# Optimization experiments

Hardware: AMD Instinct MI355X
Metric: run time of the kernel (lower is better)

## Reference

```python
import jax, jax.numpy as jnp
import numpy as np

B = 2_097_152  # batch (even, pairs are (0,1),(2,3),...)
C = 25         # hardcoded: M = eye(25), logits have 25 classes
LAMDA = 0.01


def setup_inputs() -> dict:
    key = jax.random.key(0)
    k1, k2 = jax.random.split(key, 2)
    inputs = jax.random.normal(k1, (B, C), dtype=jnp.float32)
    labels = jax.random.randint(k2, (B,), 0, C)
    M = jnp.eye(C, dtype=jnp.float32)  # learned Mahalanobis matrix (init = identity, as in torch)
    return {"inputs": inputs, "labels": labels, "M": M}


def _loss(inputs, M, labels):
    # ---- metric_learning: pairs (2i, 2i+1) ----
    a, b = inputs[0::2], inputs[1::2]          # [P, C]
    la, lb = labels[0::2], labels[1::2]        # [P]
    d = jnp.abs(a - b)                         # [P, C]
    # ||M.T * d[:,None]||_F = sqrt(sum_i d[i]^2 * sum_j M[j,i]^2)
    colsq = jnp.sum(M * M, axis=0)             # [C]
    norms = jnp.sqrt((d * d) @ colsq)          # [P]

    same = la == lb                            # positive pair mask
    pos = jnp.where(same, norms, jnp.zeros_like(norms))
    distance_p = jnp.sum(pos)
    # Faithful to source bug: distance_n is OVERWRITTEN (not accumulated) on each
    # negative pair as distance_p_so_far + norm; final value comes from the LAST
    # negative pair (0 if none exist).
    excl_cum_p = jnp.cumsum(pos) - pos         # distance_p before each pair
    neg_vals = excl_cum_p + norms              # candidate distance_n per pair
    P = norms.shape[0]
    last_neg = jnp.max(jnp.where(~same, jnp.arange(P), -1))
    distance_n = jnp.where(last_neg >= 0,
                           jnp.take(neg_vals, jnp.maximum(last_neg, 0)),
                           jnp.float32(0.0))
    metric_loss = jax.nn.relu(1.0 + distance_p - distance_n)

    # ---- cross entropy (mean over batch) ----
    logp = jax.nn.log_softmax(inputs, axis=-1)                       # [B, C]
    ce = -jnp.mean(jnp.take_along_axis(logp, labels[:, None], axis=-1))

    return ce + LAMDA * metric_loss / 2.0


def reference(inputs, labels, M):
    return _loss(inputs, M, labels)
```

## Files before the change

kernel.cpp:

```cpp
#include <hip/hip_runtime.h>
#include <math.h>

namespace {

constexpr int C      = 25;
constexpr int ROWS   = 256;
constexpr int TILE_F = ROWS * C;
constexpr int NBLK   = 512;

typedef const __attribute__((address_space(1))) void* gp_t;
typedef __attribute__((address_space(3))) void* lp_t;

__device__ __forceinline__ void load16_lds(const float* g, float* l) {
  __builtin_amdgcn_global_load_lds((gp_t)g, (lp_t)l, 16, 0, 2);
}

__global__ __launch_bounds__(256)
void k_ce(const float* __restrict__ x, const int* __restrict__ labels, int B,
          double* __restrict__ ce_part, int* __restrict__ ln_part) {
  __shared__ float tile[2][TILE_F];
  __shared__ float wsum[4];
  __shared__ int   wmax[4];

  const int t      = threadIdx.x;
  const int ntiles = B / ROWS;
  const int tpb    = ntiles / NBLK;
  const int ti0    = blockIdx.x * tpb;
  const int ti1    = min(ti0 + tpb, ntiles);

  float ce_local = 0.f;
  int   best     = -1;
  int   cur      = 0;

  int lab = 0;
  if (ti0 < ti1) {
    const float* g = x + (size_t)ti0 * TILE_F;
#pragma unroll
    for (int k = 0; k < 6; ++k)
      load16_lds(g + (k * 256 + t) * 4, &tile[0][(k * 256 + t) * 4]);
    if (t < 64) load16_lds(g + (1536 + t) * 4, &tile[0][(1536 + t) * 4]);
    lab = labels[(size_t)ti0 * ROWS + t];
  }

  for (int ti = ti0; ti < ti1; ++ti) {
    __syncthreads();

    const int tnext = ti + 1;
    int labn = 0;
    if (tnext < ti1) {
      const float* g = x + (size_t)tnext * TILE_F;
      float* buf = tile[cur ^ 1];
#pragma unroll
      for (int k = 0; k < 6; ++k)
        load16_lds(g + (k * 256 + t) * 4, &buf[(k * 256 + t) * 4]);
      if (t < 64) load16_lds(g + (1536 + t) * 4, &buf[(1536 + t) * 4]);
      labn = labels[(size_t)tnext * ROWS + t];
    }

    const float* r = &tile[cur][t * C];
    float e[C];
#pragma unroll
    for (int c = 0; c < C; ++c) e[c] = r[c];

    float m = e[0];
#pragma unroll
    for (int c = 1; c < C; ++c) m = fmaxf(m, e[c]);
    float s = 0.f, xl = 0.f;
#pragma unroll
    for (int c = 0; c < C; ++c) {
      s += __expf(e[c] - m);
      xl = (c == lab) ? e[c] : xl;
    }
    ce_local += (m + __logf(s)) - xl;

    const int nxt = __shfl_down(lab, 1, 64);
    if (((t & 1) == 0) && lab != nxt) best = ((ti * ROWS) + t) >> 1;

    lab = labn;
    cur ^= 1;
  }

#pragma unroll
  for (int off = 32; off; off >>= 1) {
    ce_local += __shfl_down(ce_local, off, 64);
    best = max(best, __shfl_down(best, off, 64));
  }
  const int lane = t & 63, wid = t >> 6;
  if (lane == 0) { wsum[wid] = ce_local; wmax[wid] = best; }
  __syncthreads();
  if (t == 0) {
    ce_part[blockIdx.x] = (double)((wsum[0] + wsum[1]) + (wsum[2] + wsum[3]));
    ln_part[blockIdx.x] = max(max(wmax[0], wmax[1]), max(wmax[2], wmax[3]));
  }
}

__global__ __launch_bounds__(256)
void k_fin(const float* __restrict__ x, const float* __restrict__ M,
           const double* __restrict__ ce_part, const int* __restrict__ ln_part,
           int P, int B, float* __restrict__ out) {
  __shared__ float  colsq[C];
  __shared__ double sred[4];
  __shared__ int    ired[4];
  __shared__ double tred[4];
  __shared__ int    s_last;

  const int t = threadIdx.x, lane = t & 63, wid = t >> 6;

  if (t < C) {
    float s = 0.f;
    for (int r = 0; r < C; ++r) {
      float m = M[r * C + t];
      s += m * m;
    }
    colsq[t] = s;
  }

  double ce = 0.0;
  int ln = -1;
  for (int i = t; i < NBLK; i += 256) {
    ce += ce_part[i];
    ln = max(ln, ln_part[i]);
  }
#pragma unroll
  for (int off = 32; off; off >>= 1) {
    ce += __shfl_down(ce, off, 64);
    ln = max(ln, __shfl_down(ln, off, 64));
  }
  if (lane == 0) { sred[wid] = ce; ired[wid] = ln; }
  __syncthreads();
  if (t == 0) s_last = max(max(ired[0], ired[1]), max(ired[2], ired[3]));
  __syncthreads();
  const int last_neg = s_last;

  double tail = 0.0;
  for (int p = last_neg + 1 + t; p < P; p += 256) {
    const float* e = x + (size_t)p * (2 * C);
    float s = 0.f;
#pragma unroll
    for (int c = 0; c < C; ++c) {
      float d = e[c] - e[C + c];
      s = fmaf(d * d, colsq[c], s);
    }
    tail += (double)sqrtf(s);
  }
  float norm_last = 0.f;
  if (t == 0 && last_neg >= 0) {
    const float* e = x + (size_t)last_neg * (2 * C);
    float s = 0.f;
#pragma unroll
    for (int c = 0; c < C; ++c) {
      float d = e[c] - e[C + c];
      s = fmaf(d * d, colsq[c], s);
    }
    norm_last = sqrtf(s);
  }
#pragma unroll
  for (int off = 32; off; off >>= 1) tail += __shfl_down(tail, off, 64);
  if (lane == 0) tred[wid] = tail;
  __syncthreads();
  if (t == 0) {
    double tl    = (tred[0] + tred[1]) + (tred[2] + tred[3]);
    double cesum = (sred[0] + sred[1]) + (sred[2] + sred[3]);
    double cem   = cesum / (double)B;
    float  ml    = fmaxf(1.0f + (float)tl - norm_last, 0.0f);
    out[0] = (float)(cem + 0.005 * (double)ml);
  }
}

}

extern "C" void kernel_launch(void* const* d_in, const int* in_sizes, int n_in,
                              void* d_out, int out_size, void* d_ws,
                              size_t ws_size, hipStream_t stream) {
  const float* x      = (const float*)d_in[0];
  const int*   labels = (const int*)d_in[1];
  const float* M      = (const float*)d_in[2];
  float*       out    = (float*)d_out;

  double* ce_part = (double*)d_ws;
  int*    ln_part = (int*)((char*)d_ws + NBLK * sizeof(double));

  const int B = in_sizes[1];
  const int P = B / 2;

  k_ce<<<NBLK, 256, 0, stream>>>(x, labels, B, ce_part, ln_part);
  k_fin<<<1, 256, 0, stream>>>(x, M, ce_part, ln_part, P, B, out);
}
```

Measured before the change: 39.76 us.

## Find last negative pair by backward label scan; accumulate CE via atomics

Replaces the two-kernel partial-sum/finalize scheme with a single-block metric kernel that scans labels backward from the end to find the last negative pair, computes the tail norms, and writes the metric term to the output first. The CE kernel then atomically adds its scaled per-block sums into the output, removing the workspace round trip and the per-row negative-pair tracking in the CE loop. The result now relies on launch ordering and float atomics, which changes summation order and gives up the double-precision final reduction.

```diff
diff --git a/kernel.cpp b/kernel.cpp
--- a/kernel.cpp
+++ b/kernel.cpp
@@ -16,11 +16,80 @@
 }
 
 __global__ __launch_bounds__(256)
+void k_metric(const float* __restrict__ x, const int* __restrict__ labels,
+              const float* __restrict__ M, int P, float* __restrict__ out) {
+  __shared__ float  colsq[C];
+  __shared__ int    sln[4];
+  __shared__ double tred[4];
+
+  const int t = threadIdx.x, lane = t & 63, wid = t >> 6;
+
+  if (t < C) {
+    float s = 0.f;
+    for (int r = 0; r < C; ++r) {
+      float m = M[r * C + t];
+      s += m * m;
+    }
+    colsq[t] = s;
+  }
+
+  int last_neg = -1;
+  for (long cs = (long)P - 256;; cs -= 256) {
+    int p = (int)cs + t;
+    int best = -1;
+    if (p >= 0 && p < P) {
+      int2 l = reinterpret_cast<const int2*>(labels)[p];
+      if (l.x != l.y) best = p;
+    }
+#pragma unroll
+    for (int off = 32; off; off >>= 1)
+      best = max(best, __shfl_down(best, off, 64));
+    if (lane == 0) sln[wid] = best;
+    __syncthreads();
+    const int bmax = max(max(sln[0], sln[1]), max(sln[2], sln[3]));
+    if (bmax >= 0 || cs <= 0) { last_neg = bmax; break; }
+    __syncthreads();
+  }
+
+  double tail = 0.0;
+  for (int p = last_neg + 1 + t; p < P; p += 256) {
+    const float* e = x + (size_t)p * (2 * C);
+    float s = 0.f;
+#pragma unroll
+    for (int c = 0; c < C; ++c) {
+      float d = e[c] - e[C + c];
+      s = fmaf(d * d, colsq[c], s);
+    }
+    tail += (double)sqrtf(s);
+  }
+#pragma unroll
+  for (int off = 32; off; off >>= 1) tail += __shfl_down(tail, off, 64);
+  if (lane == 0) tred[wid] = tail;
+  __syncthreads();
+
+  if (t == 0) {
+    float norm_last = 0.f;
+    if (last_neg >= 0) {
+      const float* e = x + (size_t)last_neg * (2 * C);
+      float s = 0.f;
+#pragma unroll
+      for (int c = 0; c < C; ++c) {
+        float d = e[c] - e[C + c];
+        s = fmaf(d * d, colsq[c], s);
+      }
+      norm_last = sqrtf(s);
+    }
+    const double tl = (tred[0] + tred[1]) + (tred[2] + tred[3]);
+    const float  ml = fmaxf(1.0f + (float)tl - norm_last, 0.0f);
+    out[0] = 0.005f * ml;
+  }
+}
+
+__global__ __launch_bounds__(256)
 void k_ce(const float* __restrict__ x, const int* __restrict__ labels, int B,
-          double* __restrict__ ce_part, int* __restrict__ ln_part) {
+          float invB, float* __restrict__ out) {
   __shared__ float tile[2][TILE_F];
   __shared__ float wsum[4];
-  __shared__ int   wmax[4];
 
   const int t      = threadIdx.x;
   const int ntiles = B / ROWS;
@@ -29,7 +98,6 @@
   const int ti1    = min(ti0 + tpb, ntiles);
 
   float ce_local = 0.f;
-  int   best     = -1;
   int   cur      = 0;
 
   int lab = 0;
@@ -73,97 +141,19 @@
     }
     ce_local += (m + __logf(s)) - xl;
 
-    const int nxt = __shfl_down(lab, 1, 64);
-    if (((t & 1) == 0) && lab != nxt) best = ((ti * ROWS) + t) >> 1;
-
     lab = labn;
     cur ^= 1;
   }
 
 #pragma unroll
-  for (int off = 32; off; off >>= 1) {
+  for (int off = 32; off; off >>= 1)
     ce_local += __shfl_down(ce_local, off, 64);
-    best = max(best, __shfl_down(best, off, 64));
-  }
   const int lane = t & 63, wid = t >> 6;
-  if (lane == 0) { wsum[wid] = ce_local; wmax[wid] = best; }
+  if (lane == 0) wsum[wid] = ce_local;
   __syncthreads();
   if (t == 0) {
-    ce_part[blockIdx.x] = (double)((wsum[0] + wsum[1]) + (wsum[2] + wsum[3]));
-    ln_part[blockIdx.x] = max(max(wmax[0], wmax[1]), max(wmax[2], wmax[3]));
-  }
-}
-
-__global__ __launch_bounds__(256)
-void k_fin(const float* __restrict__ x, const float* __restrict__ M,
-           const double* __restrict__ ce_part, const int* __restrict__ ln_part,
-           int P, int B, float* __restrict__ out) {
-  __shared__ float  colsq[C];
-  __shared__ double sred[4];
-  __shared__ int    ired[4];
-  __shared__ double tred[4];
-  __shared__ int    s_last;
-
-  const int t = threadIdx.x, lane = t & 63, wid = t >> 6;
-
-  if (t < C) {
-    float s = 0.f;
-    for (int r = 0; r < C; ++r) {
-      float m = M[r * C + t];
-      s += m * m;
-    }
-    colsq[t] = s;
-  }
-
-  double ce = 0.0;
-  int ln = -1;
-  for (int i = t; i < NBLK; i += 256) {
-    ce += ce_part[i];
-    ln = max(ln, ln_part[i]);
-  }
-#pragma unroll
-  for (int off = 32; off; off >>= 1) {
-    ce += __shfl_down(ce, off, 64);
-    ln = max(ln, __shfl_down(ln, off, 64));
-  }
-  if (lane == 0) { sred[wid] = ce; ired[wid] = ln; }
-  __syncthreads();
-  if (t == 0) s_last = max(max(ired[0], ired[1]), max(ired[2], ired[3]));
-  __syncthreads();
-  const int last_neg = s_last;
-
-  double tail = 0.0;
-  for (int p = last_neg + 1 + t; p < P; p += 256) {
-    const float* e = x + (size_t)p * (2 * C);
-    float s = 0.f;
-#pragma unroll
-    for (int c = 0; c < C; ++c) {
-      float d = e[c] - e[C + c];
-      s = fmaf(d * d, colsq[c], s);
-    }
-    tail += (double)sqrtf(s);
-  }
-  float norm_last = 0.f;
-  if (t == 0 && last_neg >= 0) {
-    const float* e = x + (size_t)last_neg * (2 * C);
-    float s = 0.f;
-#pragma unroll
-    for (int c = 0; c < C; ++c) {
-      float d = e[c] - e[C + c];
-      s = fmaf(d * d, colsq[c], s);
-    }
-    norm_last = sqrtf(s);
-  }
-#pragma unroll
-  for (int off = 32; off; off >>= 1) tail += __shfl_down(tail, off, 64);
-  if (lane == 0) tred[wid] = tail;
-  __syncthreads();
-  if (t == 0) {
-    double tl    = (tred[0] + tred[1]) + (tred[2] + tred[3]);
-    double cesum = (sred[0] + sred[1]) + (sred[2] + sred[3]);
-    double cem   = cesum / (double)B;
-    float  ml    = fmaxf(1.0f + (float)tl - norm_last, 0.0f);
-    out[0] = (float)(cem + 0.005 * (double)ml);
+    const float bs = (wsum[0] + wsum[1]) + (wsum[2] + wsum[3]);
+    atomicAdd(out, bs * invB);
   }
 }
 
@@ -177,12 +167,9 @@
   const float* M      = (const float*)d_in[2];
   float*       out    = (float*)d_out;
 
-  double* ce_part = (double*)d_ws;
-  int*    ln_part = (int*)((char*)d_ws + NBLK * sizeof(double));
-
   const int B = in_sizes[1];
   const int P = B / 2;
 
-  k_ce<<<NBLK, 256, 0, stream>>>(x, labels, B, ce_part, ln_part);
-  k_fin<<<1, 256, 0, stream>>>(x, M, ce_part, ln_part, P, B, out);
+  k_metric<<<1, 256, 0, stream>>>(x, labels, M, P, out);
+  k_ce<<<NBLK, 256, 0, stream>>>(x, labels, B, 1.0f / (float)B, out);
 }
```

After: 43.78 us. 10.1% more time.
